# Kernel tuning notes

Hardware: AMD Instinct MI355X
Metric: run time of the kernel (lower is better)

The kernel has to match this reference:

```python
import jax, jax.numpy as jnp
import numpy as np

L = 32768      # sequence length
D_MODEL = 256  # input/output feature dim
D_HIDDEN = 256 # diagonal recurrent state dim
R_MIN, R_MAX, MAX_PHASE = 0.0, 1.0, 6.28


def setup_inputs() -> dict:
    key = jax.random.key(0)
    ks = jax.random.split(key, 8)
    inputs = jax.random.normal(ks[0], (L, D_MODEL), dtype=jnp.float32)
    # nu_init: log(-0.5*log(u*(r_max^2-r_min^2)+r_min^2))
    u1 = jax.random.uniform(ks[1], (D_HIDDEN,), dtype=jnp.float32)
    nu_log = jnp.log(-0.5 * jnp.log(u1 * (R_MAX**2 - R_MIN**2) + R_MIN**2))
    # theta_init: log(max_phase*u)
    u2 = jax.random.uniform(ks[2], (D_HIDDEN,), dtype=jnp.float32)
    theta_log = jnp.log(MAX_PHASE * u2)
    # gamma_log_init from (nu_log, theta_log)
    diag_lambda = jnp.exp(-jnp.exp(nu_log) + 1j * jnp.exp(theta_log))
    gamma_log = jnp.log(jnp.sqrt(1.0 - jnp.abs(diag_lambda) ** 2))
    bnorm = np.sqrt(2 * D_MODEL).astype(np.float32) if False else jnp.sqrt(2.0 * D_MODEL)
    cnorm = jnp.sqrt(2.0 * D_HIDDEN)
    B_re = jax.random.normal(ks[3], (D_HIDDEN, D_MODEL), dtype=jnp.float32) / bnorm
    B_im = jax.random.normal(ks[4], (D_HIDDEN, D_MODEL), dtype=jnp.float32) / bnorm
    C_re = jax.random.normal(ks[5], (D_MODEL, D_HIDDEN), dtype=jnp.float32) / cnorm
    C_im = jax.random.normal(ks[6], (D_MODEL, D_HIDDEN), dtype=jnp.float32) / cnorm
    D = jax.random.normal(ks[7], (D_MODEL,), dtype=jnp.float32)
    return {"inputs": inputs, "nu_log": nu_log, "theta_log": theta_log,
            "gamma_log": gamma_log, "B_re": B_re, "B_im": B_im,
            "C_re": C_re, "C_im": C_im, "D": D}


def _binop(q_i, q_j):
    # elementwise diagonal linear-recurrence combine
    A_i, b_i = q_i
    A_j, b_j = q_j
    return (A_j * A_i, A_j * b_i + b_j)


def reference(inputs, nu_log, theta_log, gamma_log, B_re, B_im, C_re, C_im, D):
    # h_{t+1} = lambda * h_t + B_norm x_{t+1};  y_t = Re[C h_t] + D * x_t
    diag_lambda = jnp.exp(-jnp.exp(nu_log) + 1j * jnp.exp(theta_log))  # (H,)
    B_norm = (B_re + 1j * B_im) * jnp.exp(gamma_log)[:, None]          # (H, M)
    C = C_re + 1j * C_im                                               # (M, H)
    Bu = inputs.astype(B_norm.dtype) @ B_norm.T                        # (L, H) complex
    Lam = jnp.broadcast_to(diag_lambda, (inputs.shape[0], diag_lambda.shape[0]))
    _, h = jax.lax.associative_scan(_binop, (Lam, Bu))                 # (L, H)
    return jnp.real(h @ C.T) + inputs * D                              # (L, M)
```

## Files before the change

### kernel.cpp

```cpp
#include <hip/hip_runtime.h>
#include <hip/hip_bf16.h>
#include <math.h>

#define LSEQ 32768
#define DMODEL 256
#define DHID 256
#define NCH 512
#define CHUNK 128
#define NCHUNKS (LSEQ / CHUNK)

typedef __bf16 bf16_t;
typedef _Float16 f16_t;
typedef __bf16 bf16x8 __attribute__((ext_vector_type(8)));
typedef float f32x4 __attribute__((ext_vector_type(4)));

__device__ __forceinline__ void async_load16(const void* g, void* l) {
  __builtin_amdgcn_global_load_lds((__attribute__((address_space(1))) void*)g,
                                   (__attribute__((address_space(3))) void*)l,
                                   16, 0, 0);
}

__device__ __forceinline__ float f16tof(unsigned int u) {
  return (float)__builtin_bit_cast(_Float16, (unsigned short)(u & 0xffffu));
}
__device__ __forceinline__ unsigned int fTobf(float f) {
  return (unsigned int)__builtin_bit_cast(unsigned short, (bf16_t)f);
}

__global__ void prep_all(const float* __restrict__ nu_log,
                         const float* __restrict__ theta_log,
                         const float* __restrict__ gamma_log,
                         const float* __restrict__ B_re, const float* __restrict__ B_im,
                         const float* __restrict__ C_re, const float* __restrict__ C_im,
                         float* __restrict__ lam, bf16_t* __restrict__ W1,
                         bf16_t* __restrict__ W2) {
  const int bid = blockIdx.x, tid = threadIdx.x;
  if (bid == 0) {
    int h = tid;
    if (h < DHID) {
      double nu = exp((double)nu_log[h]);
      double th = exp((double)theta_log[h]);
#define PUT(row, n) { \
      double mag = exp(-(double)(n) * nu); \
      double ph  = fmod((double)(n) * th, 6.283185307179586); \
      lam[(row) * DHID + h]     = (float)(mag * cos(ph)); \
      lam[((row)+1) * DHID + h] = (float)(mag * sin(ph)); }
      PUT(0, 1.0)
      PUT(2, 32.0)
      for (int j = 0; j < 8; ++j) PUT(4 + 2 * j, 128.0 * (double)(1 << j))
#undef PUT
    }
  } else if (bid < 513) {
    int n = bid - 1, k = tid, h = n >> 1;
    float g = expf(gamma_log[h]);
    float v = (((n & 1) == 0) ? B_re[h * DMODEL + k] : B_im[h * DMODEL + k]) * g;
    W1[n * DMODEL + k] = (bf16_t)v;
  } else {
    int idx = bid - 513;
    int m = idx >> 1, k = (idx & 1) * 256 + tid, h = k >> 1;
    float v = ((k & 1) == 0) ? C_re[m * DHID + h] : -C_im[m * DHID + h];
    W2[m * NCH + k] = (bf16_t)v;
  }
}

__global__ __launch_bounds__(512) void gemm1_scan(
    const float* __restrict__ X, const bf16_t* __restrict__ Bw,
    f16_t* __restrict__ Bu, const float* __restrict__ lam,
    float* __restrict__ E) {
  __shared__ __align__(16) char smem[69632];
  bf16_t* As = (bf16_t*)smem;
  bf16_t* Bs = (bf16_t*)(smem + 8192);
  char*   Bt = smem;
  float*  Ep = (float*)(smem + 65536);

  const int tid = threadIdx.x;
  const int gx = blockIdx.x;
  const int c  = blockIdx.y;
  const int r0 = c * CHUNK;
  const int c0 = gx * 256;
  const int wave = tid >> 6, lane = tid & 63;
  const int wm = wave & 1, wn = wave >> 1;
  const int lrow = lane & 15, lk = lane >> 4;
  const int ra = tid >> 2, ka = (tid & 3) * 8;

  f32x4 acc[4][4] = {};

  for (int k0 = 0; k0 < DMODEL; k0 += 32) {
    const float* xrow = X + (size_t)(r0 + ra) * DMODEL + k0 + ka;
    float4 a0 = ((const float4*)xrow)[0];
    float4 a1 = ((const float4*)xrow)[1];
    __syncthreads();
    async_load16(Bw + (size_t)(c0 + ra) * DMODEL + k0 + ka, (char*)Bs + tid * 16);
    async_load16(Bw + (size_t)(c0 + 128 + ra) * DMODEL + k0 + ka,
                 (char*)Bs + 8192 + tid * 16);
    bf16x8 av = {(bf16_t)a0.x, (bf16_t)a0.y, (bf16_t)a0.z, (bf16_t)a0.w,
                 (bf16_t)a1.x, (bf16_t)a1.y, (bf16_t)a1.z, (bf16_t)a1.w};
    *(bf16x8*)(As + ra * 32 + ka) = av;
    __syncthreads();
    bf16x8 af[4], bfr[4];
#pragma unroll
    for (int i = 0; i < 4; ++i)
      af[i] = *(const bf16x8*)(As + (wm * 64 + i * 16 + lrow) * 32 + lk * 8);
#pragma unroll
    for (int j = 0; j < 4; ++j)
      bfr[j] = *(const bf16x8*)(Bs + (wn * 64 + j * 16 + lrow) * 32 + lk * 8);
#pragma unroll
    for (int i = 0; i < 4; ++i)
#pragma unroll
      for (int j = 0; j < 4; ++j)
        acc[i][j] = __builtin_amdgcn_mfma_f32_16x16x32_bf16(af[i], bfr[j], acc[i][j], 0, 0, 0);
  }
  __syncthreads();

#pragma unroll
  for (int i = 0; i < 4; ++i)
#pragma unroll
    for (int r = 0; r < 4; ++r) {
      int row = wm * 64 + i * 16 + lk * 4 + r;
      int key = (row & 7) << 4;
#pragma unroll
      for (int j = 0; j < 4; ++j) {
        int col = wn * 64 + j * 16 + lrow;
        *(f16_t*)(Bt + row * 512 + ((col * 2) ^ key)) = (f16_t)acc[i][j][r];
      }
    }
  __syncthreads();

  char* dst = (char*)Bu + (size_t)r0 * 1024 + gx * 512;
#pragma unroll
  for (int it = 0; it < 8; ++it) {
    int idx = it * 512 + tid;
    int row = idx >> 5, off = (idx & 31) * 16;
    *(f32x4*)(dst + (size_t)row * 1024 + off) = *(const f32x4*)(Bt + row * 512 + off);
  }

  {
    int p = tid & 127, seg = tid >> 7;
    int h = gx * 128 + p;
    float lre = lam[h], lim = lam[DHID + h];
    float sre = 0.f, sim = 0.f;
    int cb = 4 * p;
#pragma unroll 4
    for (int t = 0; t < 32; ++t) {
      int row = seg * 32 + t;
      unsigned int w = *(const unsigned int*)(Bt + row * 512 + (cb ^ ((row & 7) << 4)));
      float bre = f16tof(w), bim = f16tof(w >> 16);
      float nre = fmaf(lre, sre, fmaf(-lim, sim, bre));
      float nim = fmaf(lre, sim, fmaf(lim, sre, bim));
      sre = nre; sim = nim;
    }
    Ep[seg * 256 + 2 * p]     = sre;
    Ep[seg * 256 + 2 * p + 1] = sim;
  }
  __syncthreads();
  if (tid < 128) {
    int p = tid, h = gx * 128 + p;
    float ar = lam[2 * DHID + h], ai = lam[3 * DHID + h];
    float er = Ep[2 * p], ei = Ep[2 * p + 1];
#pragma unroll
    for (int s = 1; s < 4; ++s) {
      float tr = fmaf(ar, er, fmaf(-ai, ei, Ep[s * 256 + 2 * p]));
      float ti = fmaf(ar, ei, fmaf(ai, er, Ep[s * 256 + 2 * p + 1]));
      er = tr; ei = ti;
    }
    E[(size_t)c * NCH + 2 * h]     = er;
    E[(size_t)c * NCH + 2 * h + 1] = ei;
  }
}

__global__ __launch_bounds__(1024) void scan_gemm2(
    const f16_t* __restrict__ Bu, const bf16_t* __restrict__ W2,
    const float* __restrict__ lam, const float* __restrict__ E,
    const float* __restrict__ X, const float* __restrict__ Dv,
    float* __restrict__ out) {
  __shared__ __align__(16) char smem[155648];
  char*   H  = smem;
  bf16_t* Bs = (bf16_t*)(smem + 131072);
  float*  LB = (float*)(smem + 131072);
  float*  Pp = (float*)(smem + 135168);
  float*  Tt = (float*)(smem + 147456);

  const int tid = threadIdx.x;
  const int c = (int)gridDim.x - 1 - (int)blockIdx.x;
  const int r0 = c * CHUNK;

  const char* src = (const char*)Bu + (size_t)r0 * 1024;
#pragma unroll
  for (int it = 0; it < 8; ++it)
    async_load16(src + it * 16384 + tid * 16, H + it * 16384 + tid * 16);

  if (tid < 512) {
    int p = tid & 255, half = tid >> 8;
    int m = c >> 1;
    int lo = half ? m : 0, end = half ? c : m;
    float aR = lam[4 * DHID + p], aI = lam[5 * DHID + p];
    float sr = 0.f, si = 0.f;
#pragma unroll 4
    for (int k = lo; k < end; ++k) {
      float2 e = *(const float2*)(E + (size_t)k * NCH + 2 * p);
      float nr = fmaf(aR, sr, fmaf(-aI, si, e.x));
      float ni = fmaf(aR, si, fmaf(aI, sr, e.y));
      sr = nr; si = ni;
    }
    LB[half * 512 + 2 * p]     = sr;
    LB[half * 512 + 2 * p + 1] = si;
  }
  __syncthreads();

  {
    int p = tid & 255, seg = tid >> 8;
    float lre = lam[p], lim = lam[DHID + p];
    float sre = 0.f, sim = 0.f;
    int cb = 4 * p;
#pragma unroll 4
    for (int t = 0; t < 32; ++t) {
      int row = seg * 32 + t;
      unsigned int w = *(const unsigned int*)(H + row * 1024 + (cb ^ ((row & 7) << 4)));
      float bre = f16tof(w), bim = f16tof(w >> 16);
      float nre = fmaf(lre, sre, fmaf(-lim, sim, bre));
      float nim = fmaf(lre, sim, fmaf(lim, sre, bim));
      sre = nre; sim = nim;
    }
    Pp[seg * 512 + 2 * p]     = sre;
    Pp[seg * 512 + 2 * p + 1] = sim;
  }
  __syncthreads();

  if (tid < 256) {
    int p = tid;
    int lenb = c - (c >> 1);
    float pr = 1.f, pi = 0.f;
#pragma unroll
    for (int j = 0; j < 8; ++j)
      if (lenb & (1 << j)) {
        float br = lam[(4 + 2 * j) * DHID + p], bi = lam[(5 + 2 * j) * DHID + p];
        float nr = pr * br - pi * bi, ni = pr * bi + pi * br;
        pr = nr; pi = ni;
      }
    float sar = LB[2 * p], sai = LB[2 * p + 1];
    float sbr = LB[512 + 2 * p], sbi = LB[512 + 2 * p + 1];
    float tr = fmaf(pr, sar, fmaf(-pi, sai, sbr));
    float ti = fmaf(pr, sai, fmaf(pi, sar, sbi));
    float l32r = lam[2 * DHID + p], l32i = lam[3 * DHID + p];
    Tt[2 * p] = tr; Tt[2 * p + 1] = ti;
#pragma unroll
    for (int s = 1; s < 4; ++s) {
      float pR = Pp[(s - 1) * 512 + 2 * p], pI = Pp[(s - 1) * 512 + 2 * p + 1];
      float nr = fmaf(l32r, tr, fmaf(-l32i, ti, pR));
      float ni = fmaf(l32r, ti, fmaf(l32i, tr, pI));
      tr = nr; ti = ni;
      Tt[s * 512 + 2 * p] = tr; Tt[s * 512 + 2 * p + 1] = ti;
    }
  }
  __syncthreads();

  {
    int p = tid & 255, seg = tid >> 8;
    float lre = lam[p], lim = lam[DHID + p];
    float sre = Tt[seg * 512 + 2 * p], sim = Tt[seg * 512 + 2 * p + 1];
    int cb = 4 * p;
#pragma unroll 4
    for (int t = 0; t < 32; ++t) {
      int row = seg * 32 + t;
      unsigned int* ptr = (unsigned int*)(H + row * 1024 + (cb ^ ((row & 7) << 4)));
      unsigned int w = *ptr;
      float bre = f16tof(w), bim = f16tof(w >> 16);
      float nre = fmaf(lre, sre, fmaf(-lim, sim, bre));
      float nim = fmaf(lre, sim, fmaf(lim, sre, bim));
      sre = nre; sim = nim;
      *ptr = (fTobf(sim) << 16) | fTobf(sre);
    }
  }

  const int wave = tid >> 6, lane = tid & 63;
  const int wm = wave & 3, wn = wave >> 2;
  const int lrow = lane & 15, lk = lane >> 4;
  f32x4 acc[2][4] = {};
  for (int k0 = 0; k0 < NCH; k0 += 32) {
    __syncthreads();
    async_load16(W2 + (size_t)(tid >> 2) * NCH + k0 + (tid & 3) * 8,
                 (char*)Bs + tid * 16);
    __syncthreads();
    bf16x8 af[2], bfr[4];
#pragma unroll
    for (int i = 0; i < 2; ++i) {
      int m = wm * 32 + i * 16 + lrow;
      af[i] = *(const bf16x8*)(H + m * 1024 + ((2 * k0 + lk * 16) ^ ((m & 7) << 4)));
    }
#pragma unroll
    for (int j = 0; j < 4; ++j)
      bfr[j] = *(const bf16x8*)(Bs + (wn * 64 + j * 16 + lrow) * 32 + lk * 8);
#pragma unroll
    for (int i = 0; i < 2; ++i)
#pragma unroll
      for (int j = 0; j < 4; ++j)
        acc[i][j] = __builtin_amdgcn_mfma_f32_16x16x32_bf16(af[i], bfr[j], acc[i][j], 0, 0, 0);
  }

#pragma unroll
  for (int i = 0; i < 2; ++i)
#pragma unroll
    for (int r = 0; r < 4; ++r) {
      int row = r0 + wm * 32 + i * 16 + lk * 4 + r;
#pragma unroll
      for (int j = 0; j < 4; ++j) {
        int col = wn * 64 + j * 16 + lrow;
        float v = acc[i][j][r] + X[(size_t)row * DMODEL + col] * Dv[col];
        out[(size_t)row * DMODEL + col] = v;
      }
    }
}

extern "C" void kernel_launch(void* const* d_in, const int* in_sizes, int n_in,
                              void* d_out, int out_size, void* d_ws, size_t ws_size,
                              hipStream_t stream) {
  const float* inputs    = (const float*)d_in[0];
  const float* nu_log    = (const float*)d_in[1];
  const float* theta_log = (const float*)d_in[2];
  const float* gamma_log = (const float*)d_in[3];
  const float* B_re      = (const float*)d_in[4];
  const float* B_im      = (const float*)d_in[5];
  const float* C_re      = (const float*)d_in[6];
  const float* C_im      = (const float*)d_in[7];
  const float* Dvec      = (const float*)d_in[8];
  float* out = (float*)d_out;

  char* w = (char*)d_ws;
  bf16_t* W1 = (bf16_t*)w; w += (size_t)NCH * DMODEL * 2;
  bf16_t* W2 = (bf16_t*)w; w += (size_t)DMODEL * NCH * 2;
  float* lam = (float*)w;  w += 24576;
  f16_t* Bu  = (f16_t*)w;  w += (size_t)LSEQ * NCH * 2;
  float* E   = (float*)w;  w += (size_t)NCHUNKS * NCH * 4;

  prep_all<<<1025, 256, 0, stream>>>(nu_log, theta_log, gamma_log,
                                     B_re, B_im, C_re, C_im,
                                     lam, W1, W2);
  gemm1_scan<<<dim3(2, NCHUNKS), 512, 0, stream>>>(inputs, W1, Bu, lam, E);
  scan_gemm2<<<NCHUNKS, 1024, 0, stream>>>(Bu, W2, lam, E, inputs, Dvec, out);
}
```

Before: 155.3 us.

## Double-buffer GEMM K-loops and parallelize lambda power precompute across blocks

The first GEMM's K-loop now double-buffers its LDS tiles: the next X and W1 slices load while the current one feeds MFMA, with one barrier per step instead of two. The second GEMM stages W2 through registers with a one-step prefetch rather than a synchronous async load per step. The prep kernel spreads the ten lambda-power computations over ten blocks instead of serial double-precision work in one block. The intent is to hide global-memory latency and shorten the serial prep tail, at the cost of more registers and LDS traffic, and a launch-bounds hint that may force register spills.

```diff
diff --git a/kernel.cpp b/kernel.cpp
--- a/kernel.cpp
+++ b/kernel.cpp
@@ -35,43 +35,40 @@
                          float* __restrict__ lam, bf16_t* __restrict__ W1,
                          bf16_t* __restrict__ W2) {
   const int bid = blockIdx.x, tid = threadIdx.x;
-  if (bid == 0) {
+  if (bid < 10) {
     int h = tid;
     if (h < DHID) {
       double nu = exp((double)nu_log[h]);
       double th = exp((double)theta_log[h]);
-#define PUT(row, n) { \
-      double mag = exp(-(double)(n) * nu); \
-      double ph  = fmod((double)(n) * th, 6.283185307179586); \
-      lam[(row) * DHID + h]     = (float)(mag * cos(ph)); \
-      lam[((row)+1) * DHID + h] = (float)(mag * sin(ph)); }
-      PUT(0, 1.0)
-      PUT(2, 32.0)
-      for (int j = 0; j < 8; ++j) PUT(4 + 2 * j, 128.0 * (double)(1 << j))
-#undef PUT
-    }
-  } else if (bid < 513) {
-    int n = bid - 1, k = tid, h = n >> 1;
+      int row; double n;
+      if (bid == 0)      { row = 0; n = 1.0; }
+      else if (bid == 1) { row = 2; n = 32.0; }
+      else               { row = 4 + 2 * (bid - 2); n = 128.0 * (double)(1 << (bid - 2)); }
+      double mag = exp(-n * nu);
+      double ph  = fmod(n * th, 6.283185307179586);
+      lam[row * DHID + h]       = (float)(mag * cos(ph));
+      lam[(row + 1) * DHID + h] = (float)(mag * sin(ph));
+    }
+  } else if (bid < 522) {
+    int n = bid - 10, k = tid, h = n >> 1;
     float g = expf(gamma_log[h]);
     float v = (((n & 1) == 0) ? B_re[h * DMODEL + k] : B_im[h * DMODEL + k]) * g;
     W1[n * DMODEL + k] = (bf16_t)v;
   } else {
-    int idx = bid - 513;
+    int idx = bid - 522;
     int m = idx >> 1, k = (idx & 1) * 256 + tid, h = k >> 1;
     float v = ((k & 1) == 0) ? C_re[m * DHID + h] : -C_im[m * DHID + h];
     W2[m * NCH + k] = (bf16_t)v;
   }
 }
 
-__global__ __launch_bounds__(512) void gemm1_scan(
+__global__ __launch_bounds__(512, 4) void gemm1_scan(
     const float* __restrict__ X, const bf16_t* __restrict__ Bw,
     f16_t* __restrict__ Bu, const float* __restrict__ lam,
     float* __restrict__ E) {
   __shared__ __align__(16) char smem[69632];
-  bf16_t* As = (bf16_t*)smem;
-  bf16_t* Bs = (bf16_t*)(smem + 8192);
-  char*   Bt = smem;
-  float*  Ep = (float*)(smem + 65536);
+  char*  Bt = smem;
+  float* Ep = (float*)(smem + 65536);
 
   const int tid = threadIdx.x;
   const int gx = blockIdx.x;
@@ -85,32 +82,55 @@
 
   f32x4 acc[4][4] = {};
 
-  for (int k0 = 0; k0 < DMODEL; k0 += 32) {
-    const float* xrow = X + (size_t)(r0 + ra) * DMODEL + k0 + ka;
+  {
+    const float* xrow = X + (size_t)(r0 + ra) * DMODEL + ka;
     float4 a0 = ((const float4*)xrow)[0];
     float4 a1 = ((const float4*)xrow)[1];
-    __syncthreads();
-    async_load16(Bw + (size_t)(c0 + ra) * DMODEL + k0 + ka, (char*)Bs + tid * 16);
-    async_load16(Bw + (size_t)(c0 + 128 + ra) * DMODEL + k0 + ka,
-                 (char*)Bs + 8192 + tid * 16);
+    async_load16(Bw + (size_t)(c0 + ra) * DMODEL + ka, smem + 8192 + tid * 16);
+    async_load16(Bw + (size_t)(c0 + 128 + ra) * DMODEL + ka, smem + 16384 + tid * 16);
     bf16x8 av = {(bf16_t)a0.x, (bf16_t)a0.y, (bf16_t)a0.z, (bf16_t)a0.w,
                  (bf16_t)a1.x, (bf16_t)a1.y, (bf16_t)a1.z, (bf16_t)a1.w};
-    *(bf16x8*)(As + ra * 32 + ka) = av;
-    __syncthreads();
+    *(bf16x8*)(smem + ra * 64 + ka * 2) = av;
+  }
+  asm volatile("s_waitcnt vmcnt(0) lgkmcnt(0)" ::: "memory");
+  __builtin_amdgcn_s_barrier();
+
+#pragma unroll
+  for (int t = 0; t < 8; ++t) {
+    const int cur = t & 1, nxt = cur ^ 1;
+    const char* Asc = smem + cur * 24576;
+    const char* Bsc = smem + 8192 + cur * 24576;
+    float4 a0, a1;
+    if (t < 7) {
+      const int k0n = (t + 1) * 32;
+      const float* xrow = X + (size_t)(r0 + ra) * DMODEL + k0n + ka;
+      a0 = ((const float4*)xrow)[0];
+      a1 = ((const float4*)xrow)[1];
+      async_load16(Bw + (size_t)(c0 + ra) * DMODEL + k0n + ka,
+                   smem + 8192 + nxt * 24576 + tid * 16);
+      async_load16(Bw + (size_t)(c0 + 128 + ra) * DMODEL + k0n + ka,
+                   smem + 16384 + nxt * 24576 + tid * 16);
+    }
     bf16x8 af[4], bfr[4];
 #pragma unroll
     for (int i = 0; i < 4; ++i)
-      af[i] = *(const bf16x8*)(As + (wm * 64 + i * 16 + lrow) * 32 + lk * 8);
+      af[i] = *(const bf16x8*)(Asc + (wm * 64 + i * 16 + lrow) * 64 + lk * 16);
 #pragma unroll
     for (int j = 0; j < 4; ++j)
-      bfr[j] = *(const bf16x8*)(Bs + (wn * 64 + j * 16 + lrow) * 32 + lk * 8);
+      bfr[j] = *(const bf16x8*)(Bsc + (wn * 64 + j * 16 + lrow) * 64 + lk * 16);
 #pragma unroll
     for (int i = 0; i < 4; ++i)
 #pragma unroll
       for (int j = 0; j < 4; ++j)
         acc[i][j] = __builtin_amdgcn_mfma_f32_16x16x32_bf16(af[i], bfr[j], acc[i][j], 0, 0, 0);
-  }
-  __syncthreads();
+    if (t < 7) {
+      bf16x8 av = {(bf16_t)a0.x, (bf16_t)a0.y, (bf16_t)a0.z, (bf16_t)a0.w,
+                   (bf16_t)a1.x, (bf16_t)a1.y, (bf16_t)a1.z, (bf16_t)a1.w};
+      *(bf16x8*)(smem + nxt * 24576 + ra * 64 + ka * 2) = av;
+    }
+    asm volatile("s_waitcnt vmcnt(0) lgkmcnt(0)" ::: "memory");
+    __builtin_amdgcn_s_barrier();
+  }
 
 #pragma unroll
   for (int i = 0; i < 4; ++i)
@@ -188,6 +208,10 @@
 #pragma unroll
   for (int it = 0; it < 8; ++it)
     async_load16(src + it * 16384 + tid * 16, H + it * 16384 + tid * 16);
+
+  const char* w2src = (const char*)W2 + (size_t)(tid >> 2) * (NCH * 2) + (tid & 3) * 16;
+  f32x4 wreg[2];
+  wreg[0] = *(const f32x4*)(w2src);
 
   if (tid < 512) {
     int p = tid & 255, half = tid >> 8;
@@ -271,16 +295,20 @@
       *ptr = (fTobf(sim) << 16) | fTobf(sre);
     }
   }
+  __syncthreads();
 
   const int wave = tid >> 6, lane = tid & 63;
   const int wm = wave & 3, wn = wave >> 2;
   const int lrow = lane & 15, lk = lane >> 4;
+  *(f32x4*)((char*)Bs + tid * 16) = wreg[0];
+  wreg[1] = *(const f32x4*)(w2src + 64);
+  asm volatile("s_waitcnt lgkmcnt(0)" ::: "memory");
+  __builtin_amdgcn_s_barrier();
+
   f32x4 acc[2][4] = {};
-  for (int k0 = 0; k0 < NCH; k0 += 32) {
-    __syncthreads();
-    async_load16(W2 + (size_t)(tid >> 2) * NCH + k0 + (tid & 3) * 8,
-                 (char*)Bs + tid * 16);
-    __syncthreads();
+#pragma unroll
+  for (int t = 0; t < 16; ++t) {
+    const int k0 = t * 32;
     bf16x8 af[2], bfr[4];
 #pragma unroll
     for (int i = 0; i < 2; ++i) {
@@ -295,6 +323,13 @@
 #pragma unroll
       for (int j = 0; j < 4; ++j)
         acc[i][j] = __builtin_amdgcn_mfma_f32_16x16x32_bf16(af[i], bfr[j], acc[i][j], 0, 0, 0);
+    if (t < 15) {
+      __builtin_amdgcn_s_barrier();
+      *(f32x4*)((char*)Bs + tid * 16) = wreg[(t + 1) & 1];
+      if (t < 14) wreg[t & 1] = *(const f32x4*)(w2src + 64 * (t + 2));
+      asm volatile("s_waitcnt lgkmcnt(0)" ::: "memory");
+      __builtin_amdgcn_s_barrier();
+    }
   }
 
 #pragma unroll
@@ -332,7 +367,7 @@
   f16_t* Bu  = (f16_t*)w;  w += (size_t)LSEQ * NCH * 2;
   float* E   = (float*)w;  w += (size_t)NCHUNKS * NCH * 4;
 
-  prep_all<<<1025, 256, 0, stream>>>(nu_log, theta_log, gamma_log,
+  prep_all<<<1034, 256, 0, stream>>>(nu_log, theta_log, gamma_log,
                                      B_re, B_im, C_re, C_im,
                                      lam, W1, W2);
   gemm1_scan<<<dim3(2, NCHUNKS), 512, 0, stream>>>(inputs, W1, Bu, lam, E);
```

Result: faster. 148.3 us (-4.5%).
